# Kernel optimization log

Measured on AMD Instinct MI355X. Metric: run time of the kernel, lower is better.

## Reference

```python
import jax, jax.numpy as jnp
import numpy as np

N = 20000      # nodes
E = 320000     # edges (before self-loops)
IN = 128       # in_features
H = 8          # heads
C = 120        # out channels per head
SLOPE = 0.2    # LeakyReLU negative slope (PyG default)


def setup_inputs() -> dict:
    key = jax.random.key(0)
    k = jax.random.split(key, 8)
    x = jax.random.normal(k[0], (N, IN), jnp.float32)
    edge_index = jax.random.randint(k[1], (2, E), 0, N)  # [2,E], row0=src, row1=dst
    W = jax.random.normal(k[2], (IN, H * C), jnp.float32) / np.sqrt(IN)
    att_src = jax.random.normal(k[3], (H, C), jnp.float32) * 0.1
    att_dst = jax.random.normal(k[4], (H, C), jnp.float32) * 0.1
    bias = jnp.zeros((H * C,), jnp.float32)
    fc_w = jax.random.normal(k[5], (H * C, 2), jnp.float32) / np.sqrt(H * C)
    fc_b = jnp.zeros((2,), jnp.float32)
    return dict(x=x, edge_index=edge_index, W=W, att_src=att_src,
                att_dst=att_dst, bias=bias, fc_w=fc_w, fc_b=fc_b)


def reference(x, edge_index, W, att_src, att_dst, bias, fc_w, fc_b):
    n = x.shape[0]
    # add self loops (GATConv default add_self_loops=True)
    loops = jnp.arange(n, dtype=edge_index.dtype)
    ei = jnp.concatenate([edge_index, jnp.stack([loops, loops])], axis=1)
    src, dst = ei[0], ei[1]
    # per-head linear projection: [n, H, C]
    xp = (x @ W).reshape(n, H, C)
    # per-node attention logits
    a_s = jnp.einsum('nhc,hc->nh', xp, att_src)  # [n,H]
    a_d = jnp.einsum('nhc,hc->nh', xp, att_dst)  # [n,H]
    # edge-wise logits + LeakyReLU: [Etot,H]
    e = jax.nn.leaky_relu(a_s[src] + a_d[dst], SLOPE)
    # segment softmax over incoming edges of each destination node
    emax = jax.lax.stop_gradient(jax.ops.segment_max(e, dst, num_segments=n))
    ee = jnp.exp(e - emax[dst])
    denom = jax.ops.segment_sum(ee, dst, num_segments=n)
    alpha = ee / denom[dst]                      # [Etot,H]
    # scatter-aggregate weighted messages: [n,H,C]
    out = jax.ops.segment_sum(alpha[:, :, None] * xp[src], dst, num_segments=n)
    out = out.reshape(n, H * C) + bias           # concat heads + bias
    return out @ fc_w + fc_b                     # final Linear -> [n,2]
```

## Files before the change

kernel.cpp:

```cpp
#include <hip/hip_runtime.h>

#define NN    20000
#define EDGES 320000
#define HH    8
#define CC    120
#define HC    960
#define SLOPE 0.2f
#define BUCKET 64


__global__ __launch_bounds__(256) void prep_kernel(const float* __restrict__ W,
                                                   const float* __restrict__ att_src,
                                                   const float* __restrict__ att_dst,
                                                   const float* __restrict__ bias,
                                                   const float* __restrict__ fc_w,
                                                   const float* __restrict__ fc_b,
                                                   float* __restrict__ U,
                                                   float* __restrict__ cbias,
                                                   unsigned* __restrict__ cnt) {
  int t = threadIdx.x, b = blockIdx.x;
  int gid = b * 256 + t;
  if (gid < NN) cnt[gid] = 0u;

  int l = t & 63;
  if (b < 256) {
    int p = b * 4 + (t >> 6);
    int k = p >> 3, h = p & 7;
    const float* wrow = W + (size_t)k * HC + h * CC;
    const float* asv  = att_src + h * CC;
    const float* adv  = att_dst + h * CC;
    const float2* fv  = (const float2*)fc_w + h * CC;
    bool tail = (l < CC - 64);
    float w0 = wrow[l],            w1 = tail ? wrow[64 + l] : 0.f;
    float s0 = asv[l],             s1 = tail ? asv[64 + l] : 0.f;
    float d0 = adv[l],             d1 = tail ? adv[64 + l] : 0.f;
    float2 f0 = fv[l];
    float2 f1 = tail ? fv[64 + l] : make_float2(0.f, 0.f);
    float a_s = w0 * s0 + w1 * s1;
    float a_d = w0 * d0 + w1 * d1;
    float z0  = w0 * f0.x + w1 * f1.x;
    float z1  = w0 * f0.y + w1 * f1.y;
#pragma unroll
    for (int m = 1; m < 64; m <<= 1) {
      a_s += __shfl_xor(a_s, m);
      a_d += __shfl_xor(a_d, m);
      z0  += __shfl_xor(z0, m);
      z1  += __shfl_xor(z1, m);
    }
    if (l == 0) {
      float* u = U + k * 32 + 4 * h;
      u[0] = a_s; u[1] = z0; u[2] = z1; u[3] = a_d;
    }
  } else if (t < 128) {
    int j = t >> 6;
    float acc = 0.f;
    for (int m = l; m < HC; m += 64) acc = fmaf(bias[m], fc_w[m * 2 + j], acc);
#pragma unroll
    for (int m = 1; m < 64; m <<= 1) acc += __shfl_xor(acc, m);
    if (l == 0) cbias[j] = acc + fc_b[j];
  }
}

__global__ __launch_bounds__(256) void projscatter_kernel(const float* __restrict__ x,
                                                          const float* __restrict__ U,
                                                          const int* __restrict__ ei,
                                                          unsigned* __restrict__ cnt,
                                                          unsigned* __restrict__ list,
                                                          float* __restrict__ P) {
  __shared__ float4 xs4[256];
  __shared__ float4 Us4[1024];
  int t = threadIdx.x;
  int g = blockIdx.x * 256 + t;
  int n0 = blockIdx.x * 8;

  float4 xv  = ((const float4*)(x + (size_t)n0 * 128))[t];
  const float4* U4 = (const float4*)U;
  float4 uv0 = U4[t];
  float4 uv1 = U4[t + 256];
  float4 uv2 = U4[t + 512];
  float4 uv3 = U4[t + 768];

  if (g < EDGES) {
    int s = ei[g];
    int d = ei[EDGES + g];
    unsigned slot = atomicAdd(&cnt[d], 1u);
    list[(size_t)d * BUCKET + slot] = (unsigned)s;
  }

  xs4[t] = xv;
  Us4[t] = uv0; Us4[t + 256] = uv1; Us4[t + 512] = uv2; Us4[t + 768] = uv3;
  __syncthreads();

  int r = t >> 5, c = t & 31;
  float acc = 0.f;
  const float4* xrow = xs4 + r * 32;
  const float* Us = (const float*)Us4;
#pragma unroll 8
  for (int k4 = 0; k4 < 32; ++k4) {
    float4 v = xrow[k4];
    acc = fmaf(v.x, Us[(k4 * 4 + 0) * 32 + c], acc);
    acc = fmaf(v.y, Us[(k4 * 4 + 1) * 32 + c], acc);
    acc = fmaf(v.z, Us[(k4 * 4 + 2) * 32 + c], acc);
    acc = fmaf(v.w, Us[(k4 * 4 + 3) * 32 + c], acc);
  }
  P[(size_t)(n0 + r) * 32 + c] = acc;
}

__global__ __launch_bounds__(256) void gather_kernel(const unsigned* __restrict__ cnt,
                                                     const unsigned* __restrict__ list,
                                                     const float* __restrict__ P,
                                                     const float* __restrict__ cbias,
                                                     float* __restrict__ out) {
  int t = threadIdx.x;
  int wave = t >> 6;
  int lane = t & 63;
  int h = lane & 7;
  int o = lane >> 3;
  int dst = blockIdx.x * 4 + wave;

  const float* pd = P + (size_t)dst * 32;
  float4 pd4 = *(const float4*)(pd + 4 * h);
  float ad = pd4.w;
  unsigned deg = cnt[dst];
  unsigned rv = list[(size_t)dst * BUCKET + lane];

  float accd = 0.f, acc0 = 0.f, acc1 = 0.f;
  if (o == 0) {
    float v = pd4.x + ad;
    v = (v > 0.f) ? v : SLOPE * v;
    float ex = __expf(v);
    accd = ex;
    acc0 = ex * pd4.y;
    acc1 = ex * pd4.z;
  }
  unsigned iters = (deg + 7u) >> 3;
  unsigned e = (unsigned)o;
  for (unsigned i = 0; i < iters; ++i, e += 8u) {
    unsigned src = __shfl(rv, (int)e);
    if (e < deg) {
      float4 ps4 = *(const float4*)(P + (size_t)src * 32 + 4 * h);
      float v = ps4.x + ad;
      v = (v > 0.f) ? v : SLOPE * v;
      float ex = __expf(v);
      accd += ex;
      acc0 = fmaf(ex, ps4.y, acc0);
      acc1 = fmaf(ex, ps4.z, acc1);
    }
  }
  float accd_tot = accd + __shfl_xor(accd, 8);
  accd_tot += __shfl_xor(accd_tot, 16);
  accd_tot += __shfl_xor(accd_tot, 32);
  float r0 = acc0 / accd_tot;
  float r1 = acc1 / accd_tot;
#pragma unroll
  for (int m = 1; m < 64; m <<= 1) {
    r0 += __shfl_xor(r0, m);
    r1 += __shfl_xor(r1, m);
  }
  if (lane == 0) {
    ((float2*)out)[dst] = make_float2(cbias[0] + r0, cbias[1] + r1);
  }
}

extern "C" void kernel_launch(void* const* d_in, const int* in_sizes, int n_in,
                              void* d_out, int out_size, void* d_ws, size_t ws_size,
                              hipStream_t stream) {
  const float* x       = (const float*)d_in[0];
  const int*   ei      = (const int*)d_in[1];
  const float* W       = (const float*)d_in[2];
  const float* att_src = (const float*)d_in[3];
  const float* att_dst = (const float*)d_in[4];
  const float* bias    = (const float*)d_in[5];
  const float* fc_w    = (const float*)d_in[6];
  const float* fc_b    = (const float*)d_in[7];
  float* out = (float*)d_out;

  float*    U     = (float*)d_ws;
  float*    cbias = U + 4096;
  float*    P     = U + 8192;
  unsigned* cnt   = (unsigned*)(P + (size_t)NN * 32);
  unsigned* list  = cnt + NN;

  prep_kernel<<<257, 256, 0, stream>>>(W, att_src, att_dst, bias, fc_w, fc_b, U, cbias, cnt);
  projscatter_kernel<<<NN / 8, 256, 0, stream>>>(x, U, ei, cnt, list, P);
  gather_kernel<<<NN / 4, 256, 0, stream>>>(cnt, list, P, cbias, out);
}
```

Before: 44.00 us.

## Process 32 nodes per block with register-tiled 4-output projection and padded LDS

The projection/scatter kernel now handles 32 nodes and 512 edges per block instead of 8 nodes and 256 edges, cutting the grid to a quarter. Each thread computes four outputs with float4 LDS reads, and the x tile uses a padded row stride to avoid bank conflicts. The aim is to amortise the U tile load over more nodes and raise FMA-to-load ratio. In the gather kernel two divisions are replaced by one reciprocal and two multiplies. The trade-off is fewer blocks, so less parallelism, plus more LDS per block.

Measured after the change: 41.56 us. -5.5%, faster.

```diff
diff --git a/kernel.cpp b/kernel.cpp
--- a/kernel.cpp
+++ b/kernel.cpp
@@ -61,49 +61,65 @@
   }
 }
 
+#define XSTR 132
 __global__ __launch_bounds__(256) void projscatter_kernel(const float* __restrict__ x,
                                                           const float* __restrict__ U,
                                                           const int* __restrict__ ei,
                                                           unsigned* __restrict__ cnt,
                                                           unsigned* __restrict__ list,
                                                           float* __restrict__ P) {
-  __shared__ float4 xs4[256];
-  __shared__ float4 Us4[1024];
+  __shared__ float xs[32 * XSTR];
+  __shared__ float Us[128 * 32];
   int t = threadIdx.x;
-  int g = blockIdx.x * 256 + t;
-  int n0 = blockIdx.x * 8;
-
-  float4 xv  = ((const float4*)(x + (size_t)n0 * 128))[t];
+  int b = blockIdx.x;
+  int n0 = b * 32;
+
+  const float4* xg = (const float4*)(x + (size_t)n0 * 128);
+  float4 xv0 = xg[t], xv1 = xg[t + 256], xv2 = xg[t + 512], xv3 = xg[t + 768];
   const float4* U4 = (const float4*)U;
-  float4 uv0 = U4[t];
-  float4 uv1 = U4[t + 256];
-  float4 uv2 = U4[t + 512];
-  float4 uv3 = U4[t + 768];
-
-  if (g < EDGES) {
-    int s = ei[g];
-    int d = ei[EDGES + g];
-    unsigned slot = atomicAdd(&cnt[d], 1u);
-    list[(size_t)d * BUCKET + slot] = (unsigned)s;
-  }
-
-  xs4[t] = xv;
-  Us4[t] = uv0; Us4[t + 256] = uv1; Us4[t + 512] = uv2; Us4[t + 768] = uv3;
+  float4 uv0 = U4[t], uv1 = U4[t + 256], uv2 = U4[t + 512], uv3 = U4[t + 768];
+
+  int g0 = b * 512 + t;
+  {
+    int s0 = ei[g0],        d0 = ei[EDGES + g0];
+    int s1 = ei[g0 + 256],  d1 = ei[EDGES + g0 + 256];
+    unsigned slot0 = atomicAdd(&cnt[d0], 1u);
+    unsigned slot1 = atomicAdd(&cnt[d1], 1u);
+    list[(size_t)d0 * BUCKET + slot0] = (unsigned)s0;
+    list[(size_t)d1 * BUCKET + slot1] = (unsigned)s1;
+  }
+
+  {
+    int i0 = t, i1 = t + 256, i2 = t + 512, i3 = t + 768;
+    *(float4*)(xs + (i0 >> 5) * XSTR + (i0 & 31) * 4) = xv0;
+    *(float4*)(xs + (i1 >> 5) * XSTR + (i1 & 31) * 4) = xv1;
+    *(float4*)(xs + (i2 >> 5) * XSTR + (i2 & 31) * 4) = xv2;
+    *(float4*)(xs + (i3 >> 5) * XSTR + (i3 & 31) * 4) = xv3;
+    ((float4*)Us)[t] = uv0; ((float4*)Us)[t + 256] = uv1;
+    ((float4*)Us)[t + 512] = uv2; ((float4*)Us)[t + 768] = uv3;
+  }
   __syncthreads();
 
-  int r = t >> 5, c = t & 31;
-  float acc = 0.f;
-  const float4* xrow = xs4 + r * 32;
-  const float* Us = (const float*)Us4;
-#pragma unroll 8
+  int r = t >> 3, cq = t & 7;
+  float a0 = 0.f, a1 = 0.f, a2 = 0.f, a3 = 0.f;
+  const float* xrow = xs + r * XSTR;
+#pragma unroll 4
   for (int k4 = 0; k4 < 32; ++k4) {
-    float4 v = xrow[k4];
-    acc = fmaf(v.x, Us[(k4 * 4 + 0) * 32 + c], acc);
-    acc = fmaf(v.y, Us[(k4 * 4 + 1) * 32 + c], acc);
-    acc = fmaf(v.z, Us[(k4 * 4 + 2) * 32 + c], acc);
-    acc = fmaf(v.w, Us[(k4 * 4 + 3) * 32 + c], acc);
-  }
-  P[(size_t)(n0 + r) * 32 + c] = acc;
+    float4 xv = *(const float4*)(xrow + k4 * 4);
+    float4 u0 = *(const float4*)(Us + (k4 * 4 + 0) * 32 + 4 * cq);
+    float4 u1 = *(const float4*)(Us + (k4 * 4 + 1) * 32 + 4 * cq);
+    float4 u2 = *(const float4*)(Us + (k4 * 4 + 2) * 32 + 4 * cq);
+    float4 u3 = *(const float4*)(Us + (k4 * 4 + 3) * 32 + 4 * cq);
+    a0 = fmaf(xv.x, u0.x, a0); a1 = fmaf(xv.x, u0.y, a1);
+    a2 = fmaf(xv.x, u0.z, a2); a3 = fmaf(xv.x, u0.w, a3);
+    a0 = fmaf(xv.y, u1.x, a0); a1 = fmaf(xv.y, u1.y, a1);
+    a2 = fmaf(xv.y, u1.z, a2); a3 = fmaf(xv.y, u1.w, a3);
+    a0 = fmaf(xv.z, u2.x, a0); a1 = fmaf(xv.z, u2.y, a1);
+    a2 = fmaf(xv.z, u2.z, a2); a3 = fmaf(xv.z, u2.w, a3);
+    a0 = fmaf(xv.w, u3.x, a0); a1 = fmaf(xv.w, u3.y, a1);
+    a2 = fmaf(xv.w, u3.z, a2); a3 = fmaf(xv.w, u3.w, a3);
+  }
+  *(float4*)(P + (size_t)(n0 + r) * 32 + 4 * cq) = make_float4(a0, a1, a2, a3);
 }
 
 __global__ __launch_bounds__(256) void gather_kernel(const unsigned* __restrict__ cnt,
@@ -150,8 +166,9 @@
   float accd_tot = accd + __shfl_xor(accd, 8);
   accd_tot += __shfl_xor(accd_tot, 16);
   accd_tot += __shfl_xor(accd_tot, 32);
-  float r0 = acc0 / accd_tot;
-  float r1 = acc1 / accd_tot;
+  float rcp = 1.0f / accd_tot;
+  float r0 = acc0 * rcp;
+  float r1 = acc1 * rcp;
 #pragma unroll
   for (int m = 1; m < 64; m <<= 1) {
     r0 += __shfl_xor(r0, m);
@@ -182,6 +199,6 @@
   unsigned* list  = cnt + NN;
 
   prep_kernel<<<257, 256, 0, stream>>>(W, att_src, att_dst, bias, fc_w, fc_b, U, cbias, cnt);
-  projscatter_kernel<<<NN / 8, 256, 0, stream>>>(x, U, ei, cnt, list, P);
+  projscatter_kernel<<<NN / 32, 256, 0, stream>>>(x, U, ei, cnt, list, P);
   gather_kernel<<<NN / 4, 256, 0, stream>>>(cnt, list, P, cbias, out);
 }
```
